# Performance work log

Measured on AMD Instinct MI355X. Metric: run time of the kernel, lower is better.

## Reference

```python
import jax, jax.numpy as jnp
import numpy as np

N = 100000
E = 1600000
IN_DIM = 256
HID = 64


def setup_inputs() -> dict:
    key = jax.random.key(0)
    k1, k2, k3 = jax.random.split(key, 3)
    x = jax.random.normal(k1, (N, IN_DIM), dtype=jnp.float32)
    edge_index = jax.random.randint(k2, (2, E), 0, N, dtype=jnp.int64)
    # glorot-ish init for GCNConv weight, zero bias (PyG default)
    W = jax.random.normal(k3, (IN_DIM, HID), dtype=jnp.float32) * (1.0 / np.sqrt(IN_DIM))
    b = jnp.zeros((HID,), dtype=jnp.float32)
    return {"x": x, "edge_index": edge_index, "W": W, "b": b}


def reference(x, edge_index, W, b):
    # GCNConv: out = D^{-1/2} (A + I) D^{-1/2} (X W) + b
    n = x.shape[0]
    # add self-loops
    loop = jnp.arange(n, dtype=edge_index.dtype)
    src = jnp.concatenate([edge_index[0], loop])  # [E+N]
    dst = jnp.concatenate([edge_index[1], loop])  # [E+N]
    # degree of target nodes (incl. self-loops)
    deg = jax.ops.segment_sum(jnp.ones_like(dst, dtype=x.dtype), dst, num_segments=n)
    dinv = jnp.where(deg > 0, jax.lax.rsqrt(deg), 0.0)  # deg^{-1/2}, inf->0
    norm = dinv[src] * dinv[dst]  # [E+N]
    h = x @ W  # [N, HID] transform before aggregation
    msg = h[src] * norm[:, None]  # gather + scale, [E+N, HID]
    out = jax.ops.segment_sum(msg, dst, num_segments=n)  # scatter-add
    return out + b
```

## Files before the change

kernel.cpp:

```cpp
#include <hip/hip_runtime.h>

typedef float floatx4 __attribute__((ext_vector_type(4)));
typedef short s16x8 __attribute__((ext_vector_type(8)));

#define WG 256
#define NBUCK 512
#define BSH 8
#define EBLK 512
#define CAP 8192

__device__ inline unsigned pack_bf16_rne(float a, float b) {
    unsigned ua = __float_as_uint(a), ub = __float_as_uint(b);
    ua = (ua + 0x7FFFu + ((ua >> 16) & 1u)) >> 16;
    ub = (ub + 0x7FFFu + ((ub >> 16) & 1u)) >> 16;
    return ua | (ub << 16);
}

union FragU {
    unsigned u[4];
    uint4 q;
    s16x8 v;
};

__global__ __launch_bounds__(WG) void k_packw(const float* __restrict__ W,
                                              uint4* __restrict__ wpack,
                                              int* __restrict__ cursor) {
    const int q = blockIdx.x * WG + threadIdx.x;
    if (q < NBUCK) cursor[q] = 0;
    const int kb = q >> 8, nt = (q >> 6) & 3, ln = q & 63;
    const int quad = ln >> 4, l15 = ln & 15;
    const int col = nt * 16 + l15;
    const int krow = kb * 32 + quad * 8;
    unsigned up[4];
#pragma unroll
    for (int p = 0; p < 4; p++) {
        float a = W[(krow + 2 * p) * 64 + col];
        float b2 = W[(krow + 2 * p + 1) * 64 + col];
        up[p] = pack_bf16_rne(a, b2);
    }
    uint4 pk = {up[0], up[1], up[2], up[3]};
    wpack[q] = pk;
}

__global__ __launch_bounds__(WG) void k_main(const void* __restrict__ ei, int* __restrict__ cursor,
                                             unsigned* __restrict__ ebuf, int E,
                                             const float* __restrict__ x, const uint4* __restrict__ wpack,
                                             unsigned short* __restrict__ g, int N) {
    __shared__ int hh[NBUCK];
    __shared__ int hbase[NBUCK];
    __shared__ int s32flag;
    const int t = threadIdx.x;

    if ((int)blockIdx.x < EBLK) {
        if (t == 0) s32flag = 0;
        for (int i = t; i < NBUCK; i += WG) hh[i] = 0;
        __syncthreads();
        {
            const int* w = (const int*)ei;
            int nz = 0;
            for (int j = t; j < 4096; j += WG) nz |= (w[2 * j + 1] != 0);
            if (nz) atomicOr(&s32flag, 1);
        }
        __syncthreads();
        const bool i32 = (s32flag != 0);
        const int chunk = (E + EBLK - 1) / EBLK;
        const int s = blockIdx.x * chunk;
        const int eend = min(E, s + chunk);
        if (i32) {
            const int* pd = (const int*)ei + E;
            for (int e = s + t; e < eend; e += WG) atomicAdd(&hh[pd[e] >> BSH], 1);
        } else {
            const long long* pd = (const long long*)ei + E;
            for (int e = s + t; e < eend; e += WG) atomicAdd(&hh[(int)pd[e] >> BSH], 1);
        }
        __syncthreads();
        for (int i = t; i < NBUCK; i += WG) {
            int c = hh[i];
            hbase[i] = c ? atomicAdd(&cursor[i], c) : 0;
            hh[i] = 0;
        }
        __syncthreads();
        for (int e = s + t; e < eend; e += WG) {
            int sN, dN;
            if (i32) {
                const int* p = (const int*)ei;
                sN = p[e];
                dN = p[E + e];
            } else {
                const long long* p = (const long long*)ei;
                sN = (int)p[e];
                dN = (int)p[(long long)E + e];
            }
            int bkt = dN >> BSH;
            int pos = hbase[bkt] + atomicAdd(&hh[bkt], 1);
            if (pos < CAP) ebuf[(size_t)bkt * CAP + pos] = (unsigned)sN | ((unsigned)(dN & 255) << 24);
        }
    } else {
        const int bb = blockIdx.x - EBLK;
        const int wv = t >> 6;
        const int lane = t & 63;
        const int quad = lane >> 4, l15 = lane & 15;

        long long arow = (long long)bb * 64 + wv * 16 + l15;
        if (arow >= N) arow = N - 1;
        const float* xr = x + arow * 256 + quad * 8;
        const uint4* wp = wpack + lane;

        floatx4 acc[4];
#pragma unroll
        for (int nt = 0; nt < 4; nt++) acc[nt] = 0.f;

        floatx4 xc0 = *(const floatx4*)(xr);
        floatx4 xc1 = *(const floatx4*)(xr + 4);

#pragma unroll
        for (int kb = 0; kb < 8; kb++) {
            floatx4 xn0, xn1;
            if (kb < 7) {
                xn0 = *(const floatx4*)(xr + (kb + 1) * 32);
                xn1 = *(const floatx4*)(xr + (kb + 1) * 32 + 4);
            }
            FragU b0, b1, b2, b3;
            b0.q = wp[(kb * 4 + 0) * 64];
            b1.q = wp[(kb * 4 + 1) * 64];
            b2.q = wp[(kb * 4 + 2) * 64];
            b3.q = wp[(kb * 4 + 3) * 64];
            FragU a;
            a.u[0] = pack_bf16_rne(xc0[0], xc0[1]);
            a.u[1] = pack_bf16_rne(xc0[2], xc0[3]);
            a.u[2] = pack_bf16_rne(xc1[0], xc1[1]);
            a.u[3] = pack_bf16_rne(xc1[2], xc1[3]);
            acc[0] = __builtin_amdgcn_mfma_f32_16x16x32_bf16(a.v, b0.v, acc[0], 0, 0, 0);
            acc[1] = __builtin_amdgcn_mfma_f32_16x16x32_bf16(a.v, b1.v, acc[1], 0, 0, 0);
            acc[2] = __builtin_amdgcn_mfma_f32_16x16x32_bf16(a.v, b2.v, acc[2], 0, 0, 0);
            acc[3] = __builtin_amdgcn_mfma_f32_16x16x32_bf16(a.v, b3.v, acc[3], 0, 0, 0);
            if (kb < 7) {
                xc0 = xn0;
                xc1 = xn1;
            }
        }

        const long long orow0 = (long long)bb * 64 + wv * 16 + quad * 4;
#pragma unroll
        for (int r = 0; r < 4; r++) {
            const long long orow = orow0 + r;
            if (orow < N) {
#pragma unroll
                for (int nt = 0; nt < 4; nt++) {
                    float v = acc[nt][r];
                    unsigned uv = __float_as_uint(v);
                    uv = (uv + 0x7FFFu + ((uv >> 16) & 1u)) >> 16;
                    g[orow * 64 + nt * 16 + l15] = (unsigned short)uv;
                }
            }
        }
    }
}

__global__ __launch_bounds__(WG) void k_csr(const unsigned* __restrict__ ebuf, const int* __restrict__ cursor,
                                            int* __restrict__ off, int* __restrict__ srcs,
                                            float* __restrict__ dinv, int N, int nbuse) {
    __shared__ int red[256];
    __shared__ int h[256];
    __shared__ int sc[256];
    __shared__ int cur[256];
    const int t = threadIdx.x;
    const int b = blockIdx.x;
    const int node0 = b << BSH;
    const int rows = min(256, N - node0);
    int part = 0;
    for (int i = t; i < b; i += WG) part += min(cursor[i], CAP);
    red[t] = part;
    h[t] = 0;
    __syncthreads();
    for (int d = WG / 2; d > 0; d >>= 1) {
        if (t < d) red[t] += red[t + d];
        __syncthreads();
    }
    const int ebase = red[0];
    const int cnt = min(cursor[b], CAP);
    const unsigned* eb = ebuf + (size_t)b * CAP;
    for (int j = t; j < cnt; j += WG) atomicAdd(&h[eb[j] >> 24], 1);
    __syncthreads();
    const int deg = (t < rows) ? h[t] + 1 : 0;
    sc[t] = deg;
    __syncthreads();
    for (int d = 1; d < 256; d <<= 1) {
        int a = (t >= d) ? sc[t - d] : 0;
        __syncthreads();
        sc[t] += a;
        __syncthreads();
    }
    const int basef = ebase + node0;
    const int local = sc[t] - deg;
    if (t < rows) {
        off[node0 + t] = basef + local;
        srcs[basef + local] = node0 + t;
        cur[t] = local + 1;
        dinv[node0 + t] = rsqrtf((float)deg);
    }
    if (b == nbuse - 1 && t == 0) off[N] = ebase + cnt + N;
    __syncthreads();
    for (int j = t; j < cnt; j += WG) {
        unsigned w = eb[j];
        int dl = (int)(w >> 24);
        int pos = basef + atomicAdd(&cur[dl], 1);
        srcs[pos] = (int)(w & 0xFFFFFFu);
    }
}

__global__ __launch_bounds__(WG) void k_gather(const unsigned short* __restrict__ g,
                                               const int* __restrict__ off, const int* __restrict__ srcs,
                                               const float* __restrict__ dinv, const float* __restrict__ bias,
                                               float* __restrict__ out, int N) {
    int wid = (blockIdx.x * WG + threadIdx.x) >> 6;
    int lane = threadIdx.x & 63;
    if (wid >= N) return;
    int grp = lane >> 3;
    int c8 = (lane & 7) * 8;
    int e0 = off[wid], e1 = off[wid + 1];
    float a0 = 0.f, a1 = 0.f, a2 = 0.f, a3 = 0.f, a4 = 0.f, a5 = 0.f, a6 = 0.f, a7 = 0.f;
    int e = e0 + grp;
    int s = (e < e1) ? srcs[e] : 0;
    while (e < e1) {
        int en = e + 8;
        int sn = (en < e1) ? srcs[en] : 0;
        float ds = dinv[s];
        uint4 v = *(const uint4*)(g + (long long)s * 64 + c8);
        a0 += ds * __uint_as_float(v.x << 16);
        a1 += ds * __uint_as_float(v.x & 0xFFFF0000u);
        a2 += ds * __uint_as_float(v.y << 16);
        a3 += ds * __uint_as_float(v.y & 0xFFFF0000u);
        a4 += ds * __uint_as_float(v.z << 16);
        a5 += ds * __uint_as_float(v.z & 0xFFFF0000u);
        a6 += ds * __uint_as_float(v.w << 16);
        a7 += ds * __uint_as_float(v.w & 0xFFFF0000u);
        s = sn;
        e = en;
    }
#pragma unroll
    for (int m = 8; m <= 32; m <<= 1) {
        a0 += __shfl_xor(a0, m, 64);
        a1 += __shfl_xor(a1, m, 64);
        a2 += __shfl_xor(a2, m, 64);
        a3 += __shfl_xor(a3, m, 64);
        a4 += __shfl_xor(a4, m, 64);
        a5 += __shfl_xor(a5, m, 64);
        a6 += __shfl_xor(a6, m, 64);
        a7 += __shfl_xor(a7, m, 64);
    }
    if (grp == 0) {
        float d = dinv[wid];
        const floatx4 b0 = *(const floatx4*)(bias + c8);
        const floatx4 b1 = *(const floatx4*)(bias + c8 + 4);
        floatx4 o0, o1;
        o0[0] = d * a0 + b0[0];
        o0[1] = d * a1 + b0[1];
        o0[2] = d * a2 + b0[2];
        o0[3] = d * a3 + b0[3];
        o1[0] = d * a4 + b1[0];
        o1[1] = d * a5 + b1[1];
        o1[2] = d * a6 + b1[2];
        o1[3] = d * a7 + b1[3];
        *(floatx4*)(out + (long long)wid * 64 + c8) = o0;
        *(floatx4*)(out + (long long)wid * 64 + c8 + 4) = o1;
    }
}

extern "C" void kernel_launch(void* const* d_in, const int* in_sizes, int n_in,
                              void* d_out, int out_size, void* d_ws, size_t ws_size,
                              hipStream_t stream) {
    const float* x = (const float*)d_in[0];
    const void* ei = d_in[1];
    const float* W = (const float*)d_in[2];
    const float* b = (const float*)d_in[3];
    float* out = (float*)d_out;

    const int N = in_sizes[0] / 256;
    const int E = in_sizes[1] / 2;
    const int NBUSE = (N + 255) >> BSH;
    const int GEMMB = (N + 63) / 64;

    char* ws = (char*)d_ws;
    size_t o = 0;
    auto alloc = [&](size_t bytes) -> void* {
        void* p = ws + o;
        o += (bytes + 255) & ~(size_t)255;
        return p;
    };
    float* dinv = (float*)alloc((size_t)N * 4);
    unsigned short* g = (unsigned short*)alloc((size_t)N * 64 * 2);
    unsigned* ebuf = (unsigned*)alloc((size_t)NBUSE * CAP * 4);
    int* cursor = (int*)alloc((size_t)NBUCK * 4);
    int* off = (int*)alloc((size_t)(N + 1) * 4);
    int* srcs = (int*)alloc((size_t)(E + N) * 4);
    uint4* wpack = (uint4*)alloc((size_t)2048 * 16);
    if (o > ws_size) return;

    k_packw<<<8, WG, 0, stream>>>(W, wpack, cursor);
    k_main<<<EBLK + GEMMB, WG, 0, stream>>>(ei, cursor, ebuf, E, x, wpack, g, N);
    k_csr<<<NBUSE, WG, 0, stream>>>(ebuf, cursor, off, srcs, dinv, N, NBUSE);
    k_gather<<<(N * 64 + WG - 1) / WG, WG, 0, stream>>>(g, off, srcs, dinv, b, out, N);
}
```

Baseline: 264.6 us.

## Load edges once into registers and prefetch all X rows before MFMA loop

```diff
diff --git a/kernel.cpp b/kernel.cpp
--- a/kernel.cpp
+++ b/kernel.cpp
@@ -8,6 +8,7 @@
 #define BSH 8
 #define EBLK 512
 #define CAP 8192
+#define MAXIT 16
 
 __device__ inline unsigned pack_bf16_rne(float a, float b) {
     unsigned ua = __float_as_uint(a), ub = __float_as_uint(b);
@@ -42,10 +43,10 @@
     wpack[q] = pk;
 }
 
-__global__ __launch_bounds__(WG) void k_main(const void* __restrict__ ei, int* __restrict__ cursor,
-                                             unsigned* __restrict__ ebuf, int E,
-                                             const float* __restrict__ x, const uint4* __restrict__ wpack,
-                                             unsigned short* __restrict__ g, int N) {
+__global__ __launch_bounds__(WG, 4) void k_main(const void* __restrict__ ei, int* __restrict__ cursor,
+                                                unsigned* __restrict__ ebuf, int E,
+                                                const float* __restrict__ x, const uint4* __restrict__ wpack,
+                                                unsigned short* __restrict__ g, int N) {
     __shared__ int hh[NBUCK];
     __shared__ int hbase[NBUCK];
     __shared__ int s32flag;
@@ -66,34 +67,75 @@
         const int chunk = (E + EBLK - 1) / EBLK;
         const int s = blockIdx.x * chunk;
         const int eend = min(E, s + chunk);
-        if (i32) {
-            const int* pd = (const int*)ei + E;
-            for (int e = s + t; e < eend; e += WG) atomicAdd(&hh[pd[e] >> BSH], 1);
+
+        if (chunk <= MAXIT * WG) {
+            unsigned ew[MAXIT];
+            unsigned short ebk[MAXIT];
+#pragma unroll
+            for (int i = 0; i < MAXIT; i++) {
+                const int e = s + t + i * WG;
+                ebk[i] = 0xFFFFu;
+                if (e < eend) {
+                    int sN, dN;
+                    if (i32) {
+                        const int* p = (const int*)ei;
+                        sN = p[e];
+                        dN = p[E + e];
+                    } else {
+                        const long long* p = (const long long*)ei;
+                        sN = (int)p[e];
+                        dN = (int)p[(long long)E + e];
+                    }
+                    ew[i] = (unsigned)sN | ((unsigned)(dN & 255) << 24);
+                    ebk[i] = (unsigned short)(dN >> BSH);
+                    atomicAdd(&hh[dN >> BSH], 1);
+                }
+            }
+            __syncthreads();
+            for (int i = t; i < NBUCK; i += WG) {
+                int c = hh[i];
+                hbase[i] = c ? atomicAdd(&cursor[i], c) : 0;
+                hh[i] = 0;
+            }
+            __syncthreads();
+#pragma unroll
+            for (int i = 0; i < MAXIT; i++) {
+                if (ebk[i] != 0xFFFFu) {
+                    const int bkt = ebk[i];
+                    const int pos = hbase[bkt] + atomicAdd(&hh[bkt], 1);
+                    if (pos < CAP) ebuf[(size_t)bkt * CAP + pos] = ew[i];
+                }
+            }
         } else {
-            const long long* pd = (const long long*)ei + E;
-            for (int e = s + t; e < eend; e += WG) atomicAdd(&hh[(int)pd[e] >> BSH], 1);
-        }
-        __syncthreads();
-        for (int i = t; i < NBUCK; i += WG) {
-            int c = hh[i];
-            hbase[i] = c ? atomicAdd(&cursor[i], c) : 0;
-            hh[i] = 0;
-        }
-        __syncthreads();
-        for (int e = s + t; e < eend; e += WG) {
-            int sN, dN;
             if (i32) {
-                const int* p = (const int*)ei;
-                sN = p[e];
-                dN = p[E + e];
+                const int* pd = (const int*)ei + E;
+                for (int e = s + t; e < eend; e += WG) atomicAdd(&hh[pd[e] >> BSH], 1);
             } else {
-                const long long* p = (const long long*)ei;
-                sN = (int)p[e];
-                dN = (int)p[(long long)E + e];
-            }
-            int bkt = dN >> BSH;
-            int pos = hbase[bkt] + atomicAdd(&hh[bkt], 1);
-            if (pos < CAP) ebuf[(size_t)bkt * CAP + pos] = (unsigned)sN | ((unsigned)(dN & 255) << 24);
+                const long long* pd = (const long long*)ei + E;
+                for (int e = s + t; e < eend; e += WG) atomicAdd(&hh[(int)pd[e] >> BSH], 1);
+            }
+            __syncthreads();
+            for (int i = t; i < NBUCK; i += WG) {
+                int c = hh[i];
+                hbase[i] = c ? atomicAdd(&cursor[i], c) : 0;
+                hh[i] = 0;
+            }
+            __syncthreads();
+            for (int e = s + t; e < eend; e += WG) {
+                int sN, dN;
+                if (i32) {
+                    const int* p = (const int*)ei;
+                    sN = p[e];
+                    dN = p[E + e];
+                } else {
+                    const long long* p = (const long long*)ei;
+                    sN = (int)p[e];
+                    dN = (int)p[(long long)E + e];
+                }
+                int bkt = dN >> BSH;
+                int pos = hbase[bkt] + atomicAdd(&hh[bkt], 1);
+                if (pos < CAP) ebuf[(size_t)bkt * CAP + pos] = (unsigned)sN | ((unsigned)(dN & 255) << 24);
+            }
         }
     } else {
         const int bb = blockIdx.x - EBLK;
@@ -106,37 +148,51 @@
         const float* xr = x + arow * 256 + quad * 8;
         const uint4* wp = wpack + lane;
 
+        floatx4 xv[8][2];
+#pragma unroll
+        for (int kb = 0; kb < 8; kb++) {
+            xv[kb][0] = *(const floatx4*)(xr + kb * 32);
+            xv[kb][1] = *(const floatx4*)(xr + kb * 32 + 4);
+        }
+#pragma unroll
+        for (int kb = 0; kb < 8; kb++) {
+            asm volatile("" : "+v"(xv[kb][0]), "+v"(xv[kb][1]));
+        }
+        __builtin_amdgcn_sched_barrier(0);
+
         floatx4 acc[4];
 #pragma unroll
         for (int nt = 0; nt < 4; nt++) acc[nt] = 0.f;
 
-        floatx4 xc0 = *(const floatx4*)(xr);
-        floatx4 xc1 = *(const floatx4*)(xr + 4);
+        FragU bc0, bc1, bc2, bc3;
+        bc0.q = wp[0 * 64];
+        bc1.q = wp[1 * 64];
+        bc2.q = wp[2 * 64];
+        bc3.q = wp[3 * 64];
 
 #pragma unroll
         for (int kb = 0; kb < 8; kb++) {
-            floatx4 xn0, xn1;
+            FragU bn0, bn1, bn2, bn3;
             if (kb < 7) {
-                xn0 = *(const floatx4*)(xr + (kb + 1) * 32);
-                xn1 = *(const floatx4*)(xr + (kb + 1) * 32 + 4);
-            }
-            FragU b0, b1, b2, b3;
-            b0.q = wp[(kb * 4 + 0) * 64];
-            b1.q = wp[(kb * 4 + 1) * 64];
-            b2.q = wp[(kb * 4 + 2) * 64];
-            b3.q = wp[(kb * 4 + 3) * 64];
+                bn0.q = wp[((kb + 1) * 4 + 0) * 64];
+                bn1.q = wp[((kb + 1) * 4 + 1) * 64];
+                bn2.q = wp[((kb + 1) * 4 + 2) * 64];
+                bn3.q = wp[((kb + 1) * 4 + 3) * 64];
+            }
             FragU a;
-            a.u[0] = pack_bf16_rne(xc0[0], xc0[1]);
-            a.u[1] = pack_bf16_rne(xc0[2], xc0[3]);
-            a.u[2] = pack_bf16_rne(xc1[0], xc1[1]);
-            a.u[3] = pack_bf16_rne(xc1[2], xc1[3]);
-            acc[0] = __builtin_amdgcn_mfma_f32_16x16x32_bf16(a.v, b0.v, acc[0], 0, 0, 0);
-            acc[1] = __builtin_amdgcn_mfma_f32_16x16x32_bf16(a.v, b1.v, acc[1], 0, 0, 0);
-            acc[2] = __builtin_amdgcn_mfma_f32_16x16x32_bf16(a.v, b2.v, acc[2], 0, 0, 0);
-            acc[3] = __builtin_amdgcn_mfma_f32_16x16x32_bf16(a.v, b3.v, acc[3], 0, 0, 0);
+            a.u[0] = pack_bf16_rne(xv[kb][0][0], xv[kb][0][1]);
+            a.u[1] = pack_bf16_rne(xv[kb][0][2], xv[kb][0][3]);
+            a.u[2] = pack_bf16_rne(xv[kb][1][0], xv[kb][1][1]);
+            a.u[3] = pack_bf16_rne(xv[kb][1][2], xv[kb][1][3]);
+            acc[0] = __builtin_amdgcn_mfma_f32_16x16x32_bf16(a.v, bc0.v, acc[0], 0, 0, 0);
+            acc[1] = __builtin_amdgcn_mfma_f32_16x16x32_bf16(a.v, bc1.v, acc[1], 0, 0, 0);
+            acc[2] = __builtin_amdgcn_mfma_f32_16x16x32_bf16(a.v, bc2.v, acc[2], 0, 0, 0);
+            acc[3] = __builtin_amdgcn_mfma_f32_16x16x32_bf16(a.v, bc3.v, acc[3], 0, 0, 0);
             if (kb < 7) {
-                xc0 = xn0;
-                xc1 = xn1;
+                bc0 = bn0;
+                bc1 = bn1;
+                bc2 = bn2;
+                bc3 = bn3;
             }
         }
 
```

Result: faster. 252.4 us (-4.6%).
